# Kernel optimization log

Hardware: AMD Instinct MI355X
Metric: run time of the kernel (lower is better)

The kernel has to match this reference:

```python
import jax, jax.numpy as jnp
import numpy as np

BETA = 0.25
K = 1024   # num_codebook_vectors
D = 256    # latent_dim


def setup_inputs() -> dict:
    key = jax.random.key(0)
    k1, k2 = jax.random.split(key)
    z = jax.random.normal(k1, (16, D, 64, 64), dtype=jnp.float32)
    # embedding initialized uniform(-1/K, 1/K) as in the torch module
    emb = jax.random.uniform(k2, (K, D), dtype=jnp.float32, minval=-1.0 / K, maxval=1.0 / K)
    return {"z": z, "emb": emb}


def reference(z, emb):
    sg = jax.lax.stop_gradient
    # NCHW -> NHWC
    z_nhwc = jnp.transpose(z, (0, 2, 3, 1))            # [B,H,W,D]
    zf = z_nhwc.reshape(-1, D)                          # [N,D]
    # squared euclidean distances: ||z||^2 + ||e||^2 - 2 z e^T
    d = (jnp.sum(zf * zf, axis=1, keepdims=True)
         + jnp.sum(emb * emb, axis=1)
         - 2.0 * jnp.matmul(zf, emb.T))                 # [N,K]
    min_encoding_indices = jnp.argmin(d, axis=1)        # [N] int
    z_q = emb[min_encoding_indices].reshape(z_nhwc.shape)  # [B,H,W,D]
    # loss exactly as in source (first term is zero in value, faithful)
    loss = (jnp.mean((sg(z_nhwc) - z_nhwc) ** 2)
            + BETA * jnp.mean((z_q - sg(z_nhwc)) ** 2))
    # straight-through estimator
    z_q_st = z_nhwc + sg(z_q - z_nhwc)
    out = jnp.transpose(z_q_st, (0, 3, 1, 2))           # NHWC -> NCHW
    return out, min_encoding_indices, loss
```

## Files before the change

kernel.cpp:

```cpp
#include <hip/hip_runtime.h>

#define DD 256
#define KK 1024
#define HW 4096
#define NROWSZ 65536
#define OUT_Z 16777216
#define OUT_IDX OUT_Z
#define OUT_LOSS (OUT_Z + NROWSZ)

#define MARGIN 4.5e-4f

#define WS_ESQ   0
#define WS_EH    4096
#define WS_HLIST 528384
#define WS_HCNT  790528
#define WS_LSUM  790536
#define WS_EMBT  791552
#define WS_HZ    1840128

typedef _Float16 f16x8 __attribute__((ext_vector_type(8)));
typedef float f32x4 __attribute__((ext_vector_type(4)));
union U16x8 { uint4 u; f16x8 h; };
typedef unsigned long long u64;

static __device__ __forceinline__ u64 umin64(u64 a, u64 b) { return a < b ? a : b; }
static __device__ __forceinline__ unsigned pk16(float a, float b) {
    _Float16 ha = (_Float16)a, hb = (_Float16)b;
    return (unsigned)__builtin_bit_cast(unsigned short, ha)
         | ((unsigned)__builtin_bit_cast(unsigned short, hb) << 16);
}
static __device__ __forceinline__ void gl_lds16(const void* g, void* l) {
    __builtin_amdgcn_global_load_lds(
        (const __attribute__((address_space(1))) unsigned int*)g,
        (__attribute__((address_space(3))) unsigned int*)l, 16, 0, 0);
}

__global__ void vq_prep(const float* __restrict__ emb, float* __restrict__ esq,
                        uint2* __restrict__ eh2, int* __restrict__ hcnt,
                        double* __restrict__ lsum, float* __restrict__ embT,
                        int use_embT)
{
    const int bid = blockIdx.x;
    const int t = threadIdx.x;
    if (bid == 0 && t == 0) { *hcnt = 0; *lsum = 0.0; }

    if (bid < 4) {
        int k = bid * 256 + t;
        const float* e = emb + (size_t)k * DD;
        float blk[2];
#pragma unroll
        for (int b2 = 0; b2 < 2; ++b2) {
            const float* p = e + b2 * 128;
            float r[8];
#pragma unroll
            for (int j = 0; j < 8; ++j) r[j] = __fmul_rn(p[j], p[j]);
            for (int i = 8; i < 128; i += 8) {
#pragma unroll
                for (int j = 0; j < 8; ++j)
                    r[j] = __fadd_rn(r[j], __fmul_rn(p[i + j], p[i + j]));
            }
            blk[b2] = __fadd_rn(__fadd_rn(__fadd_rn(r[0], r[1]), __fadd_rn(r[2], r[3])),
                                __fadd_rn(__fadd_rn(r[4], r[5]), __fadd_rn(r[6], r[7])));
        }
        esq[k] = __fadd_rn(blk[0], blk[1]);
    } else if (bid < 20) {
        int tid = (bid - 4) * 256 + t;
        const float4* e4 = (const float4*)emb;
#pragma unroll
        for (int i = 0; i < 16; ++i) {
            int idx = i * 4096 + tid;
            float4 v = e4[idx];
            eh2[idx] = make_uint2(pk16(v.x, v.y), pk16(v.z, v.w));
        }
    } else {
        if (!use_embT) return;
        int u = bid - 20;
        int k = u * 64 + (t >> 2);
        int c = t & 3;
        const float4* e4 = (const float4*)(emb + (size_t)k * DD);
#pragma unroll
        for (int i = 0; i < 16; ++i) {
            float4 v = e4[c * 16 + i];
            int d = c * 64 + i * 4;
            embT[(size_t)(d + 0) * KK + k] = v.x;
            embT[(size_t)(d + 1) * KK + k] = v.y;
            embT[(size_t)(d + 2) * KK + k] = v.z;
            embT[(size_t)(d + 3) * KK + k] = v.w;
        }
    }
}

__launch_bounds__(256, 2)
__global__ void vq_score(const float* __restrict__ z, const float* __restrict__ emb,
                         const _Float16* __restrict__ eh, const float* __restrict__ esq,
                         float* __restrict__ out, int* __restrict__ hlist,
                         int* __restrict__ hcnt, double* __restrict__ lsum,
                         float* __restrict__ hz, int hzcap)
{
    __shared__ __align__(16) char smem[70928];
    char* ebufc = smem + 32768;
    float* esq_s = (float*)(smem + 65536);
    uint2 (*cand)[2] = (uint2 (*)[2])(smem + 69632);
    int* idxs = (int*)(smem + 70656);
    float* wsum = (float*)(smem + 70912);
    float* er = (float*)smem;

    const int t = threadIdx.x;
    const int lane = t & 63;
    const int w = t >> 6;
    const int col = lane & 15;
    const int quad = lane >> 4;
    const int wr = w >> 1;
    const int wc = w & 1;

    const int n0 = blockIdx.x * 64;
    const int b = n0 >> 12;
    const int hw0 = n0 & (HW - 1);
    const float* zbase = z + (size_t)b * DD * HW;

    {
        const int r = t & 63, dg = t >> 6;
        const float* src = zbase + hw0 + r;
#pragma unroll
        for (int i = 0; i < 8; ++i) {
            const int d0 = dg * 64 + i * 8;
            float v0 = src[(size_t)(d0 + 0) * HW];
            float v1 = src[(size_t)(d0 + 1) * HW];
            float v2 = src[(size_t)(d0 + 2) * HW];
            float v3 = src[(size_t)(d0 + 3) * HW];
            float v4 = src[(size_t)(d0 + 4) * HW];
            float v5 = src[(size_t)(d0 + 5) * HW];
            float v6 = src[(size_t)(d0 + 6) * HW];
            float v7 = src[(size_t)(d0 + 7) * HW];
            uint4 pk = make_uint4(pk16(v0, v1), pk16(v2, v3), pk16(v4, v5), pk16(v6, v7));
            *(uint4*)(smem + r * 512 + ((d0 * 2) ^ ((r & 7) << 4))) = pk;
        }
        esq_s[t] = esq[t];
        esq_s[256 + t] = esq[256 + t];
        esq_s[512 + t] = esq[512 + t];
        esq_s[768 + t] = esq[768 + t];
    }
    __syncthreads();

    const char* ehB = (const char*)eh;
    auto stage_tile = [&](int tt, int bufsel) {
#pragma unroll
        for (int i = 0; i < 4; ++i) {
            int pbyte = (w * 4 + i) * 1024 + lane * 16;
            int soff = pbyte ^ (((pbyte >> 9) & 7) << 4);
            gl_lds16(ehB + (size_t)tt * 16384 + soff,
                     ebufc + bufsel * 16384 + (w * 4 + i) * 1024);
        }
    };
    stage_tile(0, 0);

    U16x8 af[2][8];
#pragma unroll
    for (int nt = 0; nt < 2; ++nt)
#pragma unroll
        for (int ds = 0; ds < 8; ++ds)
            af[nt][ds].u = *(const uint4*)(smem + (wr * 32 + nt * 16 + col) * 512
                                           + ((ds * 64 + quad * 16) ^ ((col & 7) << 4)));
    __syncthreads();

    unsigned t1[8], t2[8];
#pragma unroll
    for (int i = 0; i < 8; ++i) { t1[i] = 0xFFFFFFFFu; t2[i] = 0xFFFFFFFFu; }

    const int cbyte = (wc * 16 + col) * 512;
    const int swzc = (col & 7) << 4;

    for (int tt = 0; tt < 32; ++tt) {
        const int cur = tt & 1;
        if (tt + 1 < 32) stage_tile(tt + 1, cur ^ 1);

        const char* bbuf = ebufc + cur * 16384 + cbyte;
        const int code = tt * 32 + wc * 16 + col;
        const float eq1 = 1.0f + esq_s[code];

        f32x4 acc0 = (f32x4)0.0f, acc1 = (f32x4)0.0f;
#pragma unroll
        for (int ds = 0; ds < 8; ++ds) {
            U16x8 bf;
            bf.u = *(const uint4*)(bbuf + ((ds * 64 + quad * 16) ^ swzc));
            acc0 = __builtin_amdgcn_mfma_f32_16x16x32_f16(af[0][ds].h, bf.h, acc0, 0, 0, 0);
            acc1 = __builtin_amdgcn_mfma_f32_16x16x32_f16(af[1][ds].h, bf.h, acc1, 0, 0, 0);
        }
#pragma unroll
        for (int r = 0; r < 4; ++r) {
            float s0 = fmaf(-2.0f, acc0[r], eq1);
            unsigned k0 = (__float_as_uint(s0) & 0xFFFFFC00u) | (unsigned)code;
            t2[r] = min(t2[r], max(t1[r], k0));
            t1[r] = min(t1[r], k0);
            float s1 = fmaf(-2.0f, acc1[r], eq1);
            unsigned k1 = (__float_as_uint(s1) & 0xFFFFFC00u) | (unsigned)code;
            t2[4 + r] = min(t2[4 + r], max(t1[4 + r], k1));
            t1[4 + r] = min(t1[4 + r], k1);
        }
        __syncthreads();
    }

#pragma unroll
    for (int mi = 0; mi < 8; ++mi) {
        unsigned a = t1[mi], bb = t2[mi];
#pragma unroll
        for (int off = 1; off < 16; off <<= 1) {
            unsigned o1 = __shfl_xor(a, off, 16);
            unsigned o2 = __shfl_xor(bb, off, 16);
            unsigned mx = max(a, o1);
            a = min(a, o1);
            bb = min(min(bb, o2), mx);
        }
        if (col == 0)
            cand[wr * 32 + (mi >> 2) * 16 + quad * 4 + (mi & 3)][wc] = make_uint2(a, bb);
    }
    __syncthreads();

    if (t < 64) {
        uint2 c0 = cand[t][0], c1 = cand[t][1];
        unsigned mx = max(c0.x, c1.x);
        unsigned a = min(c0.x, c1.x);
        unsigned bb = min(min(c0.y, c1.y), mx);
        float s1 = __uint_as_float(a & 0xFFFFFC00u);
        float s2 = __uint_as_float(bb & 0xFFFFFC00u);
        int k1 = (int)(a & 1023u);
        if (__fsub_rn(s2, s1) > MARGIN) {
            idxs[t] = k1;
            out[OUT_IDX + n0 + t] = (float)k1;
        } else {
            int pos = atomicAdd(hcnt, 1);
            hlist[pos] = n0 + t;
            idxs[t] = -2 - pos;
        }
    }
    __syncthreads();

    {
        const int row = t >> 2;
        const int cl = t & 3;
        int idx = idxs[row];
        if (idx >= 0) {
            const float4* e4 = (const float4*)(emb + (size_t)idx * DD);
#pragma unroll
            for (int i = 0; i < 16; ++i) {
                int ch = i * 4 + cl;
                int d0 = ch * 4;
                float4 v = e4[ch];
                *(float4*)&er[row * 256 + ((d0 + row * 4) & 255)] = v;
            }
        }
    }
    __syncthreads();

    {
        const int rr = t & 63, dg = t >> 6;
        int idx = idxs[rr];
        float lacc = 0.f;
        const float* zcol = zbase + hw0 + rr;
        if (idx >= 0) {
            float* oc = out + (size_t)b * DD * HW + hw0 + rr;
#pragma unroll 4
            for (int i = 0; i < 16; ++i) {
                int d0 = dg * 64 + i * 4;
                float4 e4 = *(const float4*)&er[rr * 256 + ((d0 + rr * 4) & 255)];
                float z0 = zcol[(size_t)(d0 + 0) * HW];
                float z1 = zcol[(size_t)(d0 + 1) * HW];
                float z2 = zcol[(size_t)(d0 + 2) * HW];
                float z3 = zcol[(size_t)(d0 + 3) * HW];
                oc[(size_t)(d0 + 0) * HW] = e4.x;
                oc[(size_t)(d0 + 1) * HW] = e4.y;
                oc[(size_t)(d0 + 2) * HW] = e4.z;
                oc[(size_t)(d0 + 3) * HW] = e4.w;
                float df;
                df = e4.x - z0; lacc = fmaf(df, df, lacc);
                df = e4.y - z1; lacc = fmaf(df, df, lacc);
                df = e4.z - z2; lacc = fmaf(df, df, lacc);
                df = e4.w - z3; lacc = fmaf(df, df, lacc);
            }
        } else {
            int pos = -2 - idx;
            if (pos < hzcap) {
                float4* dst = (float4*)(hz + (size_t)pos * DD);
#pragma unroll 4
                for (int i = 0; i < 16; ++i) {
                    int d0 = dg * 64 + i * 4;
                    float4 v;
                    v.x = zcol[(size_t)(d0 + 0) * HW];
                    v.y = zcol[(size_t)(d0 + 1) * HW];
                    v.z = zcol[(size_t)(d0 + 2) * HW];
                    v.w = zcol[(size_t)(d0 + 3) * HW];
                    dst[d0 >> 2] = v;
                }
            }
        }
#pragma unroll
        for (int off = 32; off > 0; off >>= 1) lacc += __shfl_down(lacc, off, 64);
        if (lane == 0) wsum[w] = lacc;
    }
    __syncthreads();
    if (t == 0) {
        double tot = (double)wsum[0] + (double)wsum[1] + (double)wsum[2] + (double)wsum[3];
        atomicAdd(lsum, tot);
    }
}

template<int USET>
static __device__ __forceinline__ void dot_codes(const float4* __restrict__ embT4,
                                                 const float4* __restrict__ emb4,
                                                 const float4* __restrict__ zb4,
                                                 int t, float (&acc_)[8][4])
{
#pragma unroll 2
    for (int dc = 0; dc < 64; ++dc) {
        float4 e0, e1, e2, e3;
        if (USET) {
            e0 = embT4[(size_t)(dc * 4 + 0) * 256 + t];
            e1 = embT4[(size_t)(dc * 4 + 1) * 256 + t];
            e2 = embT4[(size_t)(dc * 4 + 2) * 256 + t];
            e3 = embT4[(size_t)(dc * 4 + 3) * 256 + t];
        } else {
            float4 a0 = emb4[(size_t)(4 * t + 0) * 64 + dc];
            float4 a1 = emb4[(size_t)(4 * t + 1) * 64 + dc];
            float4 a2 = emb4[(size_t)(4 * t + 2) * 64 + dc];
            float4 a3 = emb4[(size_t)(4 * t + 3) * 64 + dc];
            e0 = make_float4(a0.x, a1.x, a2.x, a3.x);
            e1 = make_float4(a0.y, a1.y, a2.y, a3.y);
            e2 = make_float4(a0.z, a1.z, a2.z, a3.z);
            e3 = make_float4(a0.w, a1.w, a2.w, a3.w);
        }
#pragma unroll
        for (int j = 0; j < 8; ++j) {
            float4 zv = zb4[j * 64 + dc];
            acc_[j][0] = fmaf(zv.x, e0.x, acc_[j][0]);
            acc_[j][1] = fmaf(zv.x, e0.y, acc_[j][1]);
            acc_[j][2] = fmaf(zv.x, e0.z, acc_[j][2]);
            acc_[j][3] = fmaf(zv.x, e0.w, acc_[j][3]);
            acc_[j][0] = fmaf(zv.y, e1.x, acc_[j][0]);
            acc_[j][1] = fmaf(zv.y, e1.y, acc_[j][1]);
            acc_[j][2] = fmaf(zv.y, e1.z, acc_[j][2]);
            acc_[j][3] = fmaf(zv.y, e1.w, acc_[j][3]);
            acc_[j][0] = fmaf(zv.z, e2.x, acc_[j][0]);
            acc_[j][1] = fmaf(zv.z, e2.y, acc_[j][1]);
            acc_[j][2] = fmaf(zv.z, e2.z, acc_[j][2]);
            acc_[j][3] = fmaf(zv.z, e2.w, acc_[j][3]);
            acc_[j][0] = fmaf(zv.w, e3.x, acc_[j][0]);
            acc_[j][1] = fmaf(zv.w, e3.y, acc_[j][1]);
            acc_[j][2] = fmaf(zv.w, e3.z, acc_[j][2]);
            acc_[j][3] = fmaf(zv.w, e3.w, acc_[j][3]);
        }
    }
}

__launch_bounds__(256)
__global__ void vq_hard(const float* __restrict__ z, const float* __restrict__ emb,
                        const float* __restrict__ embT, const float* __restrict__ esq,
                        const float* __restrict__ hz, const int* __restrict__ hlist,
                        const int* __restrict__ hcnt, float* __restrict__ out,
                        double* __restrict__ lsum, int hzcap, int use_embT)
{
    __shared__ __align__(16) float zbuf[8 * 256];
    __shared__ float chains[8][16];
    __shared__ float zq_s[8];
    __shared__ int rows_s[8];
    __shared__ int idx_s[8];
    __shared__ u64 red[4][8];
    __shared__ float wsum[4];

    const int t = threadIdx.x;
    const int lane = t & 63;
    const int w = t >> 6;
    const int count = *hcnt;
    float lacc = 0.f;

    const float4* embT4 = (const float4*)embT;
    const float4* emb4 = (const float4*)emb;
    const float4* hz4 = (const float4*)hz;
    const float4* zb4 = (const float4*)zbuf;
    const float4 eqv4 = ((const float4*)esq)[t];
    const float eqa[4] = {eqv4.x, eqv4.y, eqv4.z, eqv4.w};

    for (int g = blockIdx.x; g * 8 < count; g += gridDim.x) {
        __syncthreads();
        if (t < 8) {
            int p = g * 8 + t;
            rows_s[t] = (p < count) ? hlist[p] : -1;
        }
        __syncthreads();

        {
            const int j = t >> 5, dpos = t & 31;
            const int pos = g * 8 + j;
            const int r = rows_s[j];
            float4 v0 = make_float4(0.f, 0.f, 0.f, 0.f), v1 = v0;
            if (r >= 0) {
                if (pos < hzcap) {
                    v0 = hz4[(size_t)pos * 64 + dpos * 2];
                    v1 = hz4[(size_t)pos * 64 + dpos * 2 + 1];
                } else {
                    const float* zp = z + (size_t)(r >> 12) * (DD * HW) + (r & (HW - 1));
                    const int d0 = dpos * 8;
                    v0.x = zp[(size_t)(d0 + 0) * HW];
                    v0.y = zp[(size_t)(d0 + 1) * HW];
                    v0.z = zp[(size_t)(d0 + 2) * HW];
                    v0.w = zp[(size_t)(d0 + 3) * HW];
                    v1.x = zp[(size_t)(d0 + 4) * HW];
                    v1.y = zp[(size_t)(d0 + 5) * HW];
                    v1.z = zp[(size_t)(d0 + 6) * HW];
                    v1.w = zp[(size_t)(d0 + 7) * HW];
                }
            }
            *(float4*)&zbuf[j * 256 + dpos * 8] = v0;
            *(float4*)&zbuf[j * 256 + dpos * 8 + 4] = v1;
        }
        __syncthreads();

        if (t < 128) {
            int j = t >> 4, c = t & 15, b2 = c >> 3, jj = c & 7;
            const float* p = &zbuf[j * 256];
            int base = b2 * 128 + jj;
            float v = p[base];
            float acc = __fmul_rn(v, v);
            for (int i = 1; i < 16; ++i) {
                float u = p[base + i * 8];
                acc = __fadd_rn(acc, __fmul_rn(u, u));
            }
            chains[j][c] = acc;
        }
        __syncthreads();
        if (t < 8) {
            const float* c = chains[t];
            float b0 = __fadd_rn(__fadd_rn(__fadd_rn(c[0], c[1]), __fadd_rn(c[2], c[3])),
                                 __fadd_rn(__fadd_rn(c[4], c[5]), __fadd_rn(c[6], c[7])));
            float b1 = __fadd_rn(__fadd_rn(__fadd_rn(c[8], c[9]), __fadd_rn(c[10], c[11])),
                                 __fadd_rn(__fadd_rn(c[12], c[13]), __fadd_rn(c[14], c[15])));
            zq_s[t] = __fadd_rn(b0, b1);
        }
        __syncthreads();

        float acc_[8][4];
#pragma unroll
        for (int j = 0; j < 8; ++j)
#pragma unroll
            for (int kk = 0; kk < 4; ++kk) acc_[j][kk] = 0.0f;

        if (use_embT) dot_codes<1>(embT4, emb4, zb4, t, acc_);
        else          dot_codes<0>(embT4, emb4, zb4, t, acc_);

#pragma unroll
        for (int j = 0; j < 8; ++j) {
            u64 m = ~0ull;
#pragma unroll
            for (int kk = 0; kk < 4; ++kk) {
                float s = __fsub_rn(__fadd_rn(zq_s[j], eqa[kk]),
                                    __fmul_rn(2.0f, acc_[j][kk]));
                u64 p = ((u64)__float_as_uint(s) << 32) | (unsigned)(4 * t + kk);
                m = umin64(m, p);
            }
#pragma unroll
            for (int off = 1; off < 64; off <<= 1)
                m = umin64(m, __shfl_xor(m, off, 64));
            if (lane == 0) red[w][j] = m;
        }
        __syncthreads();
        if (t < 8) {
            u64 m = umin64(umin64(red[0][t], red[1][t]), umin64(red[2][t], red[3][t]));
            int ki = (int)(m & 0xffffffffu);
            idx_s[t] = ki;
            int r = rows_s[t];
            if (r >= 0) out[OUT_IDX + r] = (float)ki;
        }
        __syncthreads();

        for (int p = t; p < 2048; p += 256) {
            int j = p >> 8, d = p & 255;
            int r = rows_s[j];
            if (r >= 0) {
                float e = emb[(size_t)idx_s[j] * DD + d];
                size_t off = (size_t)(r >> 12) * (DD * HW) + (size_t)d * HW + (r & (HW - 1));
                float zv = zbuf[j * 256 + d];
                out[off] = e;
                float df = e - zv;
                lacc = fmaf(df, df, lacc);
            }
        }
    }

#pragma unroll
    for (int off = 32; off > 0; off >>= 1) lacc += __shfl_down(lacc, off, 64);
    if (lane == 0) wsum[w] = lacc;
    __syncthreads();
    if (t == 0) {
        double tot = (double)wsum[0] + (double)wsum[1] + (double)wsum[2] + (double)wsum[3];
        if (tot != 0.0) atomicAdd(lsum, tot);
    }
}

__global__ void vq_final(const double* __restrict__ lsum, float* __restrict__ out)
{
    out[OUT_LOSS] = (float)(0.25 * (lsum[0] / (double)OUT_Z));
}

extern "C" void kernel_launch(void* const* d_in, const int* in_sizes, int n_in,
                              void* d_out, int out_size, void* d_ws, size_t ws_size,
                              hipStream_t stream)
{
    const float* z = (const float*)d_in[0];
    const float* emb = (const float*)d_in[1];
    float* out = (float*)d_out;
    char* w = (char*)d_ws;

    float* esq = (float*)(w + WS_ESQ);
    _Float16* eh = (_Float16*)(w + WS_EH);
    uint2* eh2 = (uint2*)(w + WS_EH);
    int* hlist = (int*)(w + WS_HLIST);
    int* hcnt = (int*)(w + WS_HCNT);
    double* lsum = (double*)(w + WS_LSUM);
    float* embT = (float*)(w + WS_EMBT);
    float* hz = (float*)(w + WS_HZ);

    int use_embT = (ws_size >= (size_t)WS_EMBT + (size_t)DD * KK * sizeof(float)) ? 1 : 0;
    int hzcap = 0;
    if (ws_size > (size_t)WS_HZ) {
        size_t c = (ws_size - (size_t)WS_HZ) / ((size_t)DD * sizeof(float));
        hzcap = (c > (size_t)NROWSZ) ? NROWSZ : (int)c;
    }

    vq_prep<<<dim3(36), dim3(256), 0, stream>>>(emb, esq, eh2, hcnt, lsum, embT, use_embT);
    vq_score<<<dim3(1024), dim3(256), 0, stream>>>(z, emb, eh, esq, out, hlist, hcnt, lsum,
                                                   hz, hzcap);
    vq_hard<<<dim3(1024), dim3(256), 0, stream>>>(z, emb, embT, esq, hz, hlist, hcnt, out,
                                                  lsum, hzcap, use_embT);
    vq_final<<<dim3(1), dim3(1), 0, stream>>>(lsum, out);
}
```

Measured before the change: 278.3 us.

## Split VQ pipeline into transpose, MFMA-fragment score, hard refine, and gather-output kernels

Adds a vq_zt kernel that transposes z into fp16 MFMA-fragment order, staging it in the output buffer, and prepacks the codebook into fragment order (ehP). vq_score can then load both operands straight into registers, with no LDS staging or per-tile barriers. Output writing and loss accumulation move out of vq_score into a new vq_out kernel. vq_out gathers from a transposed codebook held in LDS with coalesced float4 z reads and output writes, and the hz scratch buffer is removed. This costs two extra kernel launches and an extra round trip of z through memory, and it depends on the output buffer being free before the final writes.

```diff
diff --git a/kernel.cpp b/kernel.cpp
--- a/kernel.cpp
+++ b/kernel.cpp
@@ -16,7 +16,8 @@
 #define WS_HCNT  790528
 #define WS_LSUM  790536
 #define WS_EMBT  791552
-#define WS_HZ    1840128
+#define WS_EHP   1840128
+
 
 typedef _Float16 f16x8 __attribute__((ext_vector_type(8)));
 typedef float f32x4 __attribute__((ext_vector_type(4)));
@@ -29,16 +30,11 @@
     return (unsigned)__builtin_bit_cast(unsigned short, ha)
          | ((unsigned)__builtin_bit_cast(unsigned short, hb) << 16);
 }
-static __device__ __forceinline__ void gl_lds16(const void* g, void* l) {
-    __builtin_amdgcn_global_load_lds(
-        (const __attribute__((address_space(1))) unsigned int*)g,
-        (__attribute__((address_space(3))) unsigned int*)l, 16, 0, 0);
-}
 
 __global__ void vq_prep(const float* __restrict__ emb, float* __restrict__ esq,
                         uint2* __restrict__ eh2, int* __restrict__ hcnt,
                         double* __restrict__ lsum, float* __restrict__ embT,
-                        int use_embT)
+                        int use_embT, uint4* __restrict__ ehP, int use_ehp)
 {
     const int bid = blockIdx.x;
     const int t = threadIdx.x;
@@ -72,7 +68,7 @@
             float4 v = e4[idx];
             eh2[idx] = make_uint2(pk16(v.x, v.y), pk16(v.z, v.w));
         }
-    } else {
+    } else if (bid < 36) {
         if (!use_embT) return;
         int u = bid - 20;
         int k = u * 64 + (t >> 2);
@@ -87,24 +83,81 @@
             embT[(size_t)(d + 2) * KK + k] = v.z;
             embT[(size_t)(d + 3) * KK + k] = v.w;
         }
+    } else {
+        if (!use_ehp) return;
+#pragma unroll
+        for (int it = 0; it < 8; ++it) {
+            int L = ((bid - 36) * 8 + it) * 256 + t;
+            int lane = L & 63, ds = (L >> 6) & 7, wcq = (L >> 9) & 1, tt = L >> 10;
+            int col = lane & 15, quad = lane >> 4;
+            int code = tt * 32 + wcq * 16 + col;
+            int d0 = ds * 32 + quad * 8;
+            const float* e = emb + (size_t)code * DD + d0;
+            float4 a = *(const float4*)e;
+            float4 c4 = *(const float4*)(e + 4);
+            ehP[L] = make_uint4(pk16(a.x, a.y), pk16(a.z, a.w),
+                                pk16(c4.x, c4.y), pk16(c4.z, c4.w));
+        }
+    }
+}
+
+__launch_bounds__(256)
+__global__ void vq_zt(const float* __restrict__ z, float* out)
+{
+    __shared__ __align__(16) char lt[256 * 128];
+    uint4* ztF = (uint4*)out;
+
+    const int t = threadIdx.x;
+    const int lane = t & 63;
+    const int w = t >> 6;
+    const int bid = blockIdx.x;
+    const int bb = bid >> 6;
+    const int hwt = (bid >> 2) & 15;
+    const int dt = bid & 3;
+
+    {
+        const float* src = z + ((size_t)bb * DD + dt * 64) * HW + hwt * 256 + lane * 4;
+#pragma unroll
+        for (int i = 0; i < 16; ++i) {
+            const int dd = w * 16 + i;
+            float4 v = *(const float4*)(src + (size_t)dd * HW);
+            float va[4] = {v.x, v.y, v.z, v.w};
+#pragma unroll
+            for (int c = 0; c < 4; ++c) {
+                const int hwl = lane * 4 + c;
+                const int sw = ((hwl >> 2) & 7) << 4;
+                *(_Float16*)(lt + hwl * 128 + ((dd * 2) ^ sw)) = (_Float16)va[c];
+            }
+        }
+    }
+    __syncthreads();
+
+    {
+        const size_t gt = (size_t)bb * 64 + hwt * 4 + w;
+        const int col = lane & 15, quad = lane >> 4;
+#pragma unroll
+        for (int f = 0; f < 4; ++f) {
+            const int hwl = w * 64 + f * 16 + col;
+            const int sw = ((hwl >> 2) & 7) << 4;
+#pragma unroll
+            for (int dsl = 0; dsl < 2; ++dsl) {
+                const int dloc = dsl * 32 + quad * 8;
+                uint4 val = *(const uint4*)(lt + hwl * 128 + ((dloc * 2) ^ sw));
+                ztF[((gt * 4 + f) * 8 + (dt * 2 + dsl)) * 64 + lane] = val;
+            }
+        }
     }
 }
 
 __launch_bounds__(256, 2)
-__global__ void vq_score(const float* __restrict__ z, const float* __restrict__ emb,
-                         const _Float16* __restrict__ eh, const float* __restrict__ esq,
-                         float* __restrict__ out, int* __restrict__ hlist,
-                         int* __restrict__ hcnt, double* __restrict__ lsum,
-                         float* __restrict__ hz, int hzcap)
-{
-    __shared__ __align__(16) char smem[70928];
-    char* ebufc = smem + 32768;
-    float* esq_s = (float*)(smem + 65536);
-    uint2 (*cand)[2] = (uint2 (*)[2])(smem + 69632);
-    int* idxs = (int*)(smem + 70656);
-    float* wsum = (float*)(smem + 70912);
-    float* er = (float*)smem;
-
+__global__ void vq_score(float* out, const _Float16* __restrict__ eh,
+                         const uint4* __restrict__ ehP, const float* __restrict__ esq,
+                         int* __restrict__ hlist, int* __restrict__ hcnt, int use_ehp)
+{
+    __shared__ float esq_s[1024];
+    __shared__ uint2 cand[64][2];
+
+    const uint4* ztF = (const uint4*)out;
     const int t = threadIdx.x;
     const int lane = t & 63;
     const int w = t >> 6;
@@ -113,91 +166,83 @@
     const int wr = w >> 1;
     const int wc = w & 1;
 
-    const int n0 = blockIdx.x * 64;
-    const int b = n0 >> 12;
-    const int hw0 = n0 & (HW - 1);
-    const float* zbase = z + (size_t)b * DD * HW;
-
-    {
-        const int r = t & 63, dg = t >> 6;
-        const float* src = zbase + hw0 + r;
-#pragma unroll
-        for (int i = 0; i < 8; ++i) {
-            const int d0 = dg * 64 + i * 8;
-            float v0 = src[(size_t)(d0 + 0) * HW];
-            float v1 = src[(size_t)(d0 + 1) * HW];
-            float v2 = src[(size_t)(d0 + 2) * HW];
-            float v3 = src[(size_t)(d0 + 3) * HW];
-            float v4 = src[(size_t)(d0 + 4) * HW];
-            float v5 = src[(size_t)(d0 + 5) * HW];
-            float v6 = src[(size_t)(d0 + 6) * HW];
-            float v7 = src[(size_t)(d0 + 7) * HW];
-            uint4 pk = make_uint4(pk16(v0, v1), pk16(v2, v3), pk16(v4, v5), pk16(v6, v7));
-            *(uint4*)(smem + r * 512 + ((d0 * 2) ^ ((r & 7) << 4))) = pk;
-        }
-        esq_s[t] = esq[t];
-        esq_s[256 + t] = esq[256 + t];
-        esq_s[512 + t] = esq[512 + t];
-        esq_s[768 + t] = esq[768 + t];
+    const int gt = blockIdx.x;
+    const int n0 = gt * 64;
+
+    esq_s[t] = esq[t];
+    esq_s[256 + t] = esq[256 + t];
+    esq_s[512 + t] = esq[512 + t];
+    esq_s[768 + t] = esq[768 + t];
+
+    U16x8 af[2][8];
+#pragma unroll
+    for (int nt = 0; nt < 2; ++nt) {
+        const int f = wr * 2 + nt;
+#pragma unroll
+        for (int ds = 0; ds < 8; ++ds)
+            af[nt][ds].u = ztF[(((size_t)gt * 4 + f) * 8 + ds) * 64 + lane];
     }
     __syncthreads();
 
-    const char* ehB = (const char*)eh;
-    auto stage_tile = [&](int tt, int bufsel) {
-#pragma unroll
-        for (int i = 0; i < 4; ++i) {
-            int pbyte = (w * 4 + i) * 1024 + lane * 16;
-            int soff = pbyte ^ (((pbyte >> 9) & 7) << 4);
-            gl_lds16(ehB + (size_t)tt * 16384 + soff,
-                     ebufc + bufsel * 16384 + (w * 4 + i) * 1024);
-        }
-    };
-    stage_tile(0, 0);
-
-    U16x8 af[2][8];
-#pragma unroll
-    for (int nt = 0; nt < 2; ++nt)
-#pragma unroll
-        for (int ds = 0; ds < 8; ++ds)
-            af[nt][ds].u = *(const uint4*)(smem + (wr * 32 + nt * 16 + col) * 512
-                                           + ((ds * 64 + quad * 16) ^ ((col & 7) << 4)));
-    __syncthreads();
-
     unsigned t1[8], t2[8];
 #pragma unroll
     for (int i = 0; i < 8; ++i) { t1[i] = 0xFFFFFFFFu; t2[i] = 0xFFFFFFFFu; }
 
-    const int cbyte = (wc * 16 + col) * 512;
-    const int swzc = (col & 7) << 4;
-
-    for (int tt = 0; tt < 32; ++tt) {
-        const int cur = tt & 1;
-        if (tt + 1 < 32) stage_tile(tt + 1, cur ^ 1);
-
-        const char* bbuf = ebufc + cur * 16384 + cbyte;
-        const int code = tt * 32 + wc * 16 + col;
-        const float eq1 = 1.0f + esq_s[code];
-
-        f32x4 acc0 = (f32x4)0.0f, acc1 = (f32x4)0.0f;
-#pragma unroll
-        for (int ds = 0; ds < 8; ++ds) {
-            U16x8 bf;
-            bf.u = *(const uint4*)(bbuf + ((ds * 64 + quad * 16) ^ swzc));
-            acc0 = __builtin_amdgcn_mfma_f32_16x16x32_f16(af[0][ds].h, bf.h, acc0, 0, 0, 0);
-            acc1 = __builtin_amdgcn_mfma_f32_16x16x32_f16(af[1][ds].h, bf.h, acc1, 0, 0, 0);
-        }
-#pragma unroll
-        for (int r = 0; r < 4; ++r) {
-            float s0 = fmaf(-2.0f, acc0[r], eq1);
-            unsigned k0 = (__float_as_uint(s0) & 0xFFFFFC00u) | (unsigned)code;
-            t2[r] = min(t2[r], max(t1[r], k0));
-            t1[r] = min(t1[r], k0);
-            float s1 = fmaf(-2.0f, acc1[r], eq1);
-            unsigned k1 = (__float_as_uint(s1) & 0xFFFFFC00u) | (unsigned)code;
-            t2[4 + r] = min(t2[4 + r], max(t1[4 + r], k1));
-            t1[4 + r] = min(t1[4 + r], k1);
-        }
-        __syncthreads();
+    if (use_ehp) {
+        const uint4* bp = ehP + (size_t)wc * 512 + lane;
+#pragma unroll 2
+        for (int tt = 0; tt < 32; ++tt) {
+            const uint4* p = bp + (size_t)tt * 1024;
+            U16x8 bf[8];
+#pragma unroll
+            for (int ds = 0; ds < 8; ++ds) bf[ds].u = p[ds * 64];
+            const int code = tt * 32 + wc * 16 + col;
+            const float eq1 = 1.0f + esq_s[code];
+            f32x4 acc0 = (f32x4)0.0f, acc1 = (f32x4)0.0f;
+#pragma unroll
+            for (int ds = 0; ds < 8; ++ds) {
+                acc0 = __builtin_amdgcn_mfma_f32_16x16x32_f16(af[0][ds].h, bf[ds].h, acc0, 0, 0, 0);
+                acc1 = __builtin_amdgcn_mfma_f32_16x16x32_f16(af[1][ds].h, bf[ds].h, acc1, 0, 0, 0);
+            }
+#pragma unroll
+            for (int r = 0; r < 4; ++r) {
+                float s0 = fmaf(-2.0f, acc0[r], eq1);
+                unsigned k0 = (__float_as_uint(s0) & 0xFFFFFC00u) | (unsigned)code;
+                t2[r] = min(t2[r], max(t1[r], k0));
+                t1[r] = min(t1[r], k0);
+                float s1 = fmaf(-2.0f, acc1[r], eq1);
+                unsigned k1 = (__float_as_uint(s1) & 0xFFFFFC00u) | (unsigned)code;
+                t2[4 + r] = min(t2[4 + r], max(t1[4 + r], k1));
+                t1[4 + r] = min(t1[4 + r], k1);
+            }
+        }
+    } else {
+        const uint4* ehq = (const uint4*)eh;
+        for (int tt = 0; tt < 32; ++tt) {
+            const int code = tt * 32 + wc * 16 + col;
+            const uint4* bp = ehq + (size_t)code * 32 + quad;
+            U16x8 bf[8];
+#pragma unroll
+            for (int ds = 0; ds < 8; ++ds) bf[ds].u = bp[ds * 4];
+            const float eq1 = 1.0f + esq_s[code];
+            f32x4 acc0 = (f32x4)0.0f, acc1 = (f32x4)0.0f;
+#pragma unroll
+            for (int ds = 0; ds < 8; ++ds) {
+                acc0 = __builtin_amdgcn_mfma_f32_16x16x32_f16(af[0][ds].h, bf[ds].h, acc0, 0, 0, 0);
+                acc1 = __builtin_amdgcn_mfma_f32_16x16x32_f16(af[1][ds].h, bf[ds].h, acc1, 0, 0, 0);
+            }
+#pragma unroll
+            for (int r = 0; r < 4; ++r) {
+                float s0 = fmaf(-2.0f, acc0[r], eq1);
+                unsigned k0 = (__float_as_uint(s0) & 0xFFFFFC00u) | (unsigned)code;
+                t2[r] = min(t2[r], max(t1[r], k0));
+                t1[r] = min(t1[r], k0);
+                float s1 = fmaf(-2.0f, acc1[r], eq1);
+                unsigned k1 = (__float_as_uint(s1) & 0xFFFFFC00u) | (unsigned)code;
+                t2[4 + r] = min(t2[4 + r], max(t1[4 + r], k1));
+                t1[4 + r] = min(t1[4 + r], k1);
+            }
+        }
     }
 
 #pragma unroll
@@ -225,82 +270,11 @@
         float s2 = __uint_as_float(bb & 0xFFFFFC00u);
         int k1 = (int)(a & 1023u);
         if (__fsub_rn(s2, s1) > MARGIN) {
-            idxs[t] = k1;
             out[OUT_IDX + n0 + t] = (float)k1;
         } else {
             int pos = atomicAdd(hcnt, 1);
             hlist[pos] = n0 + t;
-            idxs[t] = -2 - pos;
-        }
-    }
-    __syncthreads();
-
-    {
-        const int row = t >> 2;
-        const int cl = t & 3;
-        int idx = idxs[row];
-        if (idx >= 0) {
-            const float4* e4 = (const float4*)(emb + (size_t)idx * DD);
-#pragma unroll
-            for (int i = 0; i < 16; ++i) {
-                int ch = i * 4 + cl;
-                int d0 = ch * 4;
-                float4 v = e4[ch];
-                *(float4*)&er[row * 256 + ((d0 + row * 4) & 255)] = v;
-            }
-        }
-    }
-    __syncthreads();
-
-    {
-        const int rr = t & 63, dg = t >> 6;
-        int idx = idxs[rr];
-        float lacc = 0.f;
-        const float* zcol = zbase + hw0 + rr;
-        if (idx >= 0) {
-            float* oc = out + (size_t)b * DD * HW + hw0 + rr;
-#pragma unroll 4
-            for (int i = 0; i < 16; ++i) {
-                int d0 = dg * 64 + i * 4;
-                float4 e4 = *(const float4*)&er[rr * 256 + ((d0 + rr * 4) & 255)];
-                float z0 = zcol[(size_t)(d0 + 0) * HW];
-                float z1 = zcol[(size_t)(d0 + 1) * HW];
-                float z2 = zcol[(size_t)(d0 + 2) * HW];
-                float z3 = zcol[(size_t)(d0 + 3) * HW];
-                oc[(size_t)(d0 + 0) * HW] = e4.x;
-                oc[(size_t)(d0 + 1) * HW] = e4.y;
-                oc[(size_t)(d0 + 2) * HW] = e4.z;
-                oc[(size_t)(d0 + 3) * HW] = e4.w;
-                float df;
-                df = e4.x - z0; lacc = fmaf(df, df, lacc);
-                df = e4.y - z1; lacc = fmaf(df, df, lacc);
-                df = e4.z - z2; lacc = fmaf(df, df, lacc);
-                df = e4.w - z3; lacc = fmaf(df, df, lacc);
-            }
-        } else {
-            int pos = -2 - idx;
-            if (pos < hzcap) {
-                float4* dst = (float4*)(hz + (size_t)pos * DD);
-#pragma unroll 4
-                for (int i = 0; i < 16; ++i) {
-                    int d0 = dg * 64 + i * 4;
-                    float4 v;
-                    v.x = zcol[(size_t)(d0 + 0) * HW];
-                    v.y = zcol[(size_t)(d0 + 1) * HW];
-                    v.z = zcol[(size_t)(d0 + 2) * HW];
-                    v.w = zcol[(size_t)(d0 + 3) * HW];
-                    dst[d0 >> 2] = v;
-                }
-            }
-        }
-#pragma unroll
-        for (int off = 32; off > 0; off >>= 1) lacc += __shfl_down(lacc, off, 64);
-        if (lane == 0) wsum[w] = lacc;
-    }
-    __syncthreads();
-    if (t == 0) {
-        double tot = (double)wsum[0] + (double)wsum[1] + (double)wsum[2] + (double)wsum[3];
-        atomicAdd(lsum, tot);
+        }
     }
 }
 
@@ -354,27 +328,22 @@
 __launch_bounds__(256)
 __global__ void vq_hard(const float* __restrict__ z, const float* __restrict__ emb,
                         const float* __restrict__ embT, const float* __restrict__ esq,
-                        const float* __restrict__ hz, const int* __restrict__ hlist,
-                        const int* __restrict__ hcnt, float* __restrict__ out,
-                        double* __restrict__ lsum, int hzcap, int use_embT)
+                        const int* __restrict__ hlist, const int* __restrict__ hcnt,
+                        float* __restrict__ out, int use_embT)
 {
     __shared__ __align__(16) float zbuf[8 * 256];
     __shared__ float chains[8][16];
     __shared__ float zq_s[8];
     __shared__ int rows_s[8];
-    __shared__ int idx_s[8];
     __shared__ u64 red[4][8];
-    __shared__ float wsum[4];
 
     const int t = threadIdx.x;
     const int lane = t & 63;
     const int w = t >> 6;
     const int count = *hcnt;
-    float lacc = 0.f;
 
     const float4* embT4 = (const float4*)embT;
     const float4* emb4 = (const float4*)emb;
-    const float4* hz4 = (const float4*)hz;
     const float4* zb4 = (const float4*)zbuf;
     const float4 eqv4 = ((const float4*)esq)[t];
     const float eqa[4] = {eqv4.x, eqv4.y, eqv4.z, eqv4.w};
@@ -389,25 +358,19 @@
 
         {
             const int j = t >> 5, dpos = t & 31;
-            const int pos = g * 8 + j;
             const int r = rows_s[j];
             float4 v0 = make_float4(0.f, 0.f, 0.f, 0.f), v1 = v0;
             if (r >= 0) {
-                if (pos < hzcap) {
-                    v0 = hz4[(size_t)pos * 64 + dpos * 2];
-                    v1 = hz4[(size_t)pos * 64 + dpos * 2 + 1];
-                } else {
-                    const float* zp = z + (size_t)(r >> 12) * (DD * HW) + (r & (HW - 1));
-                    const int d0 = dpos * 8;
-                    v0.x = zp[(size_t)(d0 + 0) * HW];
-                    v0.y = zp[(size_t)(d0 + 1) * HW];
-                    v0.z = zp[(size_t)(d0 + 2) * HW];
-                    v0.w = zp[(size_t)(d0 + 3) * HW];
-                    v1.x = zp[(size_t)(d0 + 4) * HW];
-                    v1.y = zp[(size_t)(d0 + 5) * HW];
-                    v1.z = zp[(size_t)(d0 + 6) * HW];
-                    v1.w = zp[(size_t)(d0 + 7) * HW];
-                }
+                const float* zp = z + (size_t)(r >> 12) * (DD * HW) + (r & (HW - 1));
+                const int d0 = dpos * 8;
+                v0.x = zp[(size_t)(d0 + 0) * HW];
+                v0.y = zp[(size_t)(d0 + 1) * HW];
+                v0.z = zp[(size_t)(d0 + 2) * HW];
+                v0.w = zp[(size_t)(d0 + 3) * HW];
+                v1.x = zp[(size_t)(d0 + 4) * HW];
+                v1.y = zp[(size_t)(d0 + 5) * HW];
+                v1.z = zp[(size_t)(d0 + 6) * HW];
+                v1.w = zp[(size_t)(d0 + 7) * HW];
             }
             *(float4*)&zbuf[j * 256 + dpos * 8] = v0;
             *(float4*)&zbuf[j * 256 + dpos * 8 + 4] = v1;
@@ -464,34 +427,71 @@
         __syncthreads();
         if (t < 8) {
             u64 m = umin64(umin64(red[0][t], red[1][t]), umin64(red[2][t], red[3][t]));
-            int ki = (int)(m & 0xffffffffu);
-            idx_s[t] = ki;
             int r = rows_s[t];
-            if (r >= 0) out[OUT_IDX + r] = (float)ki;
-        }
-        __syncthreads();
-
-        for (int p = t; p < 2048; p += 256) {
-            int j = p >> 8, d = p & 255;
-            int r = rows_s[j];
-            if (r >= 0) {
-                float e = emb[(size_t)idx_s[j] * DD + d];
-                size_t off = (size_t)(r >> 12) * (DD * HW) + (size_t)d * HW + (r & (HW - 1));
-                float zv = zbuf[j * 256 + d];
-                out[off] = e;
-                float df = e - zv;
-                lacc = fmaf(df, df, lacc);
-            }
-        }
-    }
-
+            if (r >= 0) out[OUT_IDX + r] = (float)(int)(m & 0xffffffffu);
+        }
+    }
+}
+
+__launch_bounds__(256)
+__global__ void vq_out(const float* __restrict__ z, const float* __restrict__ emb,
+                       const float* __restrict__ embT, float* out,
+                       double* __restrict__ lsum, int use_embT)
+{
+    __shared__ float et[8 * 1024];
+    __shared__ float wsum[4];
+
+    const int t = threadIdx.x;
+    const int lane = t & 63;
+    const int w = t >> 6;
+    const int bb = blockIdx.x >> 5;
+    const int dg = blockIdx.x & 31;
+
+    if (use_embT) {
+#pragma unroll
+        for (int c = 0; c < 8; ++c)
+            *(float4*)&et[c * 1024 + t * 4] =
+                *(const float4*)&embT[(size_t)(dg * 8 + c) * KK + t * 4];
+    } else {
+        for (int i = 0; i < 32; ++i) {
+            int kk = i * 256 + t;
+            et[kk] = emb[(size_t)(kk & 1023) * DD + dg * 8 + (kk >> 10)];
+        }
+    }
+    __syncthreads();
+
+    float lacc = 0.f;
+    const size_t zb = (size_t)bb * DD * HW;
+    const float* idxf = out + OUT_IDX + (size_t)bb * HW;
+#pragma unroll
+    for (int ch = 0; ch < 4; ++ch) {
+        const int hw = ch * 1024 + t * 4;
+        float4 fi = *(const float4*)&idxf[hw];
+        int k0 = (int)fi.x, k1 = (int)fi.y, k2 = (int)fi.z, k3 = (int)fi.w;
+#pragma unroll
+        for (int dl = 0; dl < 8; ++dl) {
+            size_t off = zb + (size_t)(dg * 8 + dl) * HW + hw;
+            float4 zv = *(const float4*)&z[off];
+            float4 e;
+            e.x = et[dl * 1024 + k0];
+            e.y = et[dl * 1024 + k1];
+            e.z = et[dl * 1024 + k2];
+            e.w = et[dl * 1024 + k3];
+            *(float4*)&out[off] = e;
+            float df;
+            df = e.x - zv.x; lacc = fmaf(df, df, lacc);
+            df = e.y - zv.y; lacc = fmaf(df, df, lacc);
+            df = e.z - zv.z; lacc = fmaf(df, df, lacc);
+            df = e.w - zv.w; lacc = fmaf(df, df, lacc);
+        }
+    }
 #pragma unroll
     for (int off = 32; off > 0; off >>= 1) lacc += __shfl_down(lacc, off, 64);
     if (lane == 0) wsum[w] = lacc;
     __syncthreads();
     if (t == 0) {
         double tot = (double)wsum[0] + (double)wsum[1] + (double)wsum[2] + (double)wsum[3];
-        if (tot != 0.0) atomicAdd(lsum, tot);
+        atomicAdd(lsum, tot);
     }
 }
 
@@ -516,19 +516,17 @@
     int* hcnt = (int*)(w + WS_HCNT);
     double* lsum = (double*)(w + WS_LSUM);
     float* embT = (float*)(w + WS_EMBT);
-    float* hz = (float*)(w + WS_HZ);
+    uint4* ehP = (uint4*)(w + WS_EHP);
 
     int use_embT = (ws_size >= (size_t)WS_EMBT + (size_t)DD * KK * sizeof(float)) ? 1 : 0;
-    int hzcap = 0;
-    if (ws_size > (size_t)WS_HZ) {
-        size_t c = (ws_size - (size_t)WS_HZ) / ((size_t)DD * sizeof(float));
-        hzcap = (c > (size_t)NROWSZ) ? NROWSZ : (int)c;
-    }
-
-    vq_prep<<<dim3(36), dim3(256), 0, stream>>>(emb, esq, eh2, hcnt, lsum, embT, use_embT);
-    vq_score<<<dim3(1024), dim3(256), 0, stream>>>(z, emb, eh, esq, out, hlist, hcnt, lsum,
-                                                   hz, hzcap);
-    vq_hard<<<dim3(1024), dim3(256), 0, stream>>>(z, emb, embT, esq, hz, hlist, hcnt, out,
-                                                  lsum, hzcap, use_embT);
+    int use_ehp = (ws_size >= (size_t)WS_EHP + (size_t)KK * DD * sizeof(_Float16)) ? 1 : 0;
+
+    vq_prep<<<dim3(52), dim3(256), 0, stream>>>(emb, esq, eh2, hcnt, lsum, embT, use_embT,
+                                                ehP, use_ehp);
+    vq_zt<<<dim3(1024), dim3(256), 0, stream>>>(z, out);
+    vq_score<<<dim3(1024), dim3(256), 0, stream>>>(out, eh, ehP, esq, hlist, hcnt, use_ehp);
+    vq_hard<<<dim3(1024), dim3(256), 0, stream>>>(z, emb, embT, esq, hlist, hcnt, out,
+                                                  use_embT);
+    vq_out<<<dim3(512), dim3(256), 0, stream>>>(z, emb, embT, out, lsum, use_embT);
     vq_final<<<dim3(1), dim3(1), 0, stream>>>(lsum, out);
 }
```

After: 271.9 us. -2.3%, faster.
